# Optimization experiments

Hardware: AMD Instinct MI355X
Metric: run time of the kernel (lower is better)

## Reference

```python
import jax, jax.numpy as jnp
import numpy as np


def setup_inputs() -> dict:
    key = jax.random.key(0)
    k1, k2 = jax.random.split(key)
    y = jax.random.normal(k1, (2048, 256), dtype=jnp.float32)  # (num_labels, 2*hidden)
    x = jax.random.normal(k2, (1024, 128), dtype=jnp.float32)  # (batch, hidden)
    return {"y": y, "x": x}


def reference(y, x):
    h = y.shape[-1] // 2
    # box parameters: min coordinate and softplus delta
    mn = y[:, :h][None, :, :]                      # (1, L, h)
    delta = jax.nn.softplus(y[:, h:])[None, :, :]  # (1, L, h)
    mx = mn + delta
    center = mn + delta / 2.0
    dp1 = delta + 1.0
    xr = x[:, None, :]                             # (B, 1, h)
    l1 = jnp.abs(xr - center)                      # (B, L, h)
    inside = (mn <= xr) & (xr <= mx)
    outside_dist = l1 * dp1 - delta / 2.0 * (delta - 1.0 / (delta + 1e-10))
    per_dim = jnp.where(inside, l1 / (dp1 + 1e-10), outside_dist)
    distance = jnp.linalg.norm(per_dim, axis=-1)   # (B, L)
    return -distance
```

## Files before the change

kernel.cpp:

```cpp
#include <hip/hip_runtime.h>
#include <hip/hip_bf16.h>
#include <math.h>


#define BM 32
#define BN 64
#define TM 8

__global__ __launch_bounds__(256) void boxe_prep(const float* __restrict__ y,
                                                 float4* __restrict__ p4)
{
    __shared__ float t0[128][9], t1[128][9], t2[128][9], t3[128][9];
    const int tid = threadIdx.x;
    const int n0  = blockIdx.x * 8;

#pragma unroll
    for (int i = 0; i < 4; ++i) {
        int j  = i * 256 + tid;
        int k  = j & 127;
        int nl = j >> 7;
        int n  = n0 + nl;
        float mn = y[n * 256 + k];
        float dv = y[n * 256 + 128 + k];
        float delta = fmaxf(dv, 0.0f) + log1pf(expf(-fabsf(dv)));
        float hd  = 0.5f * delta;
        t0[k][nl] = mn + hd;
        t1[k][nl] = hd;
        t2[k][nl] = 1.0f / (delta + 1.0f + 1e-10f);
        t3[k][nl] = hd * (delta - 1.0f / (delta + 1e-10f));
    }
    __syncthreads();

#pragma unroll
    for (int i = 0; i < 4; ++i) {
        int j  = i * 256 + tid;
        int nl = j & 7;
        int k  = j >> 3;
        p4[k * 2048 + n0 + nl] =
            make_float4(t0[k][nl], t1[k][nl], t2[k][nl], t3[k][nl]);
    }
}

__global__ __launch_bounds__(256) void boxe_main(
    const float4* __restrict__ p4, const float* __restrict__ x,
    float* __restrict__ out)
{
    __shared__ float xtile[128][BM + 1];

    const int tid  = threadIdx.x;
    const int lane = tid & 63;
    const int wave = tid >> 6;
    const int m0   = blockIdx.y * BM;
    const int n0   = blockIdx.x * BN;

#pragma unroll
    for (int i = 0; i < (128 * BM) / 256; ++i) {
        int idx = i * 256 + tid;
        int m = idx >> 7;
        int k = idx & 127;
        xtile[k][m] = x[(m0 + m) * 128 + k];
    }
    __syncthreads();

    float acc[TM];
#pragma unroll
    for (int r = 0; r < TM; ++r) acc[r] = 0.0f;

    const int n  = n0 + lane;
    const int mw = wave * TM;

#pragma unroll 8
    for (int k = 0; k < 128; ++k) {
        float4 p = p4[k * 2048 + n];
        float dp1 = fmaf(2.0f, p.y, 1.0f);
#pragma unroll
        for (int r = 0; r < TM; ++r) {
            float xv = xtile[k][mw + r];
            float l = fabsf(xv - p.x);
            float v = (l <= p.y) ? (l * p.z) : fmaf(l, dp1, -p.w);
            acc[r] = fmaf(v, v, acc[r]);
        }
    }

#pragma unroll
    for (int r = 0; r < TM; ++r) {
        int m = m0 + mw + r;
        out[m * 2048 + n] = -sqrtf(acc[r]);
    }
}

extern "C" void kernel_launch(void* const* d_in, const int* in_sizes, int n_in,
                              void* d_out, int out_size, void* d_ws, size_t ws_size,
                              hipStream_t stream) {
    const float* y = (const float*)d_in[0];
    const float* x = (const float*)d_in[1];
    float* out = (float*)d_out;

    float4* p4 = (float4*)d_ws;

    hipLaunchKernelGGL(boxe_prep, dim3(2048 / 8), dim3(256), 0, stream, y, p4);

    dim3 grid(2048 / BN, 1024 / BM);
    hipLaunchKernelGGL(boxe_main, grid, dim3(256), 0, stream, p4, x, out);
}
```

Before: 118.1 us.

## Read x through wave-uniform scalar loads instead of an LDS tile

Drops the shared-memory staging of the x tile and its barrier. Each wave now reads its eight x rows straight from global memory with wave-uniform addresses (readfirstlane on the wave index), so the compiler can use scalar loads and SGPR operands in place of LDS reads. It also adds a launch_bounds occupancy hint of 4. The risk is scalar-cache latency on the inner loop and a register-pressure limit from the occupancy hint.

```diff
diff --git a/kernel.cpp b/kernel.cpp
--- a/kernel.cpp
+++ b/kernel.cpp
@@ -41,52 +41,60 @@
     }
 }
 
-__global__ __launch_bounds__(256) void boxe_main(
+__global__ __launch_bounds__(256, 4) void boxe_main(
     const float4* __restrict__ p4, const float* __restrict__ x,
     float* __restrict__ out)
 {
-    __shared__ float xtile[128][BM + 1];
-
     const int tid  = threadIdx.x;
     const int lane = tid & 63;
-    const int wave = tid >> 6;
-    const int m0   = blockIdx.y * BM;
-    const int n0   = blockIdx.x * BN;
+    const int wave = __builtin_amdgcn_readfirstlane(tid >> 6);
+    const int m0   = blockIdx.y * BM + wave * TM;
+    const int n    = blockIdx.x * BN + lane;
 
-#pragma unroll
-    for (int i = 0; i < (128 * BM) / 256; ++i) {
-        int idx = i * 256 + tid;
-        int m = idx >> 7;
-        int k = idx & 127;
-        xtile[k][m] = x[(m0 + m) * 128 + k];
-    }
-    __syncthreads();
+    const float* xr0 = x + (m0 + 0) * 128;
+    const float* xr1 = x + (m0 + 1) * 128;
+    const float* xr2 = x + (m0 + 2) * 128;
+    const float* xr3 = x + (m0 + 3) * 128;
+    const float* xr4 = x + (m0 + 4) * 128;
+    const float* xr5 = x + (m0 + 5) * 128;
+    const float* xr6 = x + (m0 + 6) * 128;
+    const float* xr7 = x + (m0 + 7) * 128;
 
-    float acc[TM];
-#pragma unroll
-    for (int r = 0; r < TM; ++r) acc[r] = 0.0f;
+    const float4* pp = p4 + n;
 
-    const int n  = n0 + lane;
-    const int mw = wave * TM;
+    float acc0 = 0.0f, acc1 = 0.0f, acc2 = 0.0f, acc3 = 0.0f;
+    float acc4 = 0.0f, acc5 = 0.0f, acc6 = 0.0f, acc7 = 0.0f;
+
+#define EVAL(ACC, XS)                                                     \
+    do {                                                                  \
+        float l = fabsf((XS) - p.x);                                      \
+        float v = (l <= p.y) ? (l * p.z) : fmaf(l, dp1, -p.w);            \
+        ACC = fmaf(v, v, ACC);                                            \
+    } while (0)
 
 #pragma unroll 8
     for (int k = 0; k < 128; ++k) {
-        float4 p = p4[k * 2048 + n];
+        float4 p  = pp[k * 2048];
         float dp1 = fmaf(2.0f, p.y, 1.0f);
-#pragma unroll
-        for (int r = 0; r < TM; ++r) {
-            float xv = xtile[k][mw + r];
-            float l = fabsf(xv - p.x);
-            float v = (l <= p.y) ? (l * p.z) : fmaf(l, dp1, -p.w);
-            acc[r] = fmaf(v, v, acc[r]);
-        }
+        EVAL(acc0, xr0[k]);
+        EVAL(acc1, xr1[k]);
+        EVAL(acc2, xr2[k]);
+        EVAL(acc3, xr3[k]);
+        EVAL(acc4, xr4[k]);
+        EVAL(acc5, xr5[k]);
+        EVAL(acc6, xr6[k]);
+        EVAL(acc7, xr7[k]);
     }
+#undef EVAL
 
-#pragma unroll
-    for (int r = 0; r < TM; ++r) {
-        int m = m0 + mw + r;
-        out[m * 2048 + n] = -sqrtf(acc[r]);
-    }
+    out[(m0 + 0) * 2048 + n] = -sqrtf(acc0);
+    out[(m0 + 1) * 2048 + n] = -sqrtf(acc1);
+    out[(m0 + 2) * 2048 + n] = -sqrtf(acc2);
+    out[(m0 + 3) * 2048 + n] = -sqrtf(acc3);
+    out[(m0 + 4) * 2048 + n] = -sqrtf(acc4);
+    out[(m0 + 5) * 2048 + n] = -sqrtf(acc5);
+    out[(m0 + 6) * 2048 + n] = -sqrtf(acc6);
+    out[(m0 + 7) * 2048 + n] = -sqrtf(acc7);
 }
 
 extern "C" void kernel_launch(void* const* d_in, const int* in_sizes, int n_in,
```

Result: no change. 115.8 us (-1.9%).
